# Kernel optimization log

Hardware: AMD Instinct MI355X
Metric: run time of the kernel (lower is better)

The kernel has to match this reference:

```python
import jax, jax.numpy as jnp
import numpy as np

B, C, H, W = 8, 64, 64, 64
DQK = C // 8  # q/k projection dim = 8


def setup_inputs() -> dict:
    key = jax.random.key(0)
    ks = jax.random.split(key, 5)
    return {
        "query": jax.random.normal(ks[0], (B, C, H, W), dtype=jnp.float32),
        "value": jax.random.normal(ks[1], (B, C, H, W), dtype=jnp.float32),
        "Wq": jax.random.normal(ks[2], (DQK, C), dtype=jnp.float32) * (1.0 / np.sqrt(C)),
        "bq": jnp.zeros((DQK,), dtype=jnp.float32),
        "Wk": jax.random.normal(ks[3], (DQK, C), dtype=jnp.float32) * (1.0 / np.sqrt(C)),
        "bk": jnp.zeros((DQK,), dtype=jnp.float32),
        "Wv": jax.random.normal(ks[4], (C, C), dtype=jnp.float32) * (1.0 / np.sqrt(C)),
        "bv": jnp.zeros((C,), dtype=jnp.float32),
    }


def reference(query, value, Wq, bq, Wk, bk, Wv, bv):
    b, c, h, w = value.shape
    n = h * w
    # 1x1 convs are per-pixel matmuls over channels
    q = jnp.einsum("oc,bchw->bohw", Wq, query) + bq[None, :, None, None]
    k = jnp.einsum("oc,bchw->bohw", Wk, query) + bk[None, :, None, None]
    v = jnp.einsum("oc,bchw->bohw", Wv, value) + bv[None, :, None, None]
    proj_q = q.reshape(b, DQK, n).transpose(0, 2, 1)  # [B, N, d]
    proj_k = k.reshape(b, DQK, n)                      # [B, d, N]
    energy = jnp.einsum("bnd,bdm->bnm", proj_q, proj_k)  # [B, N, N]
    attention = jax.nn.softmax(energy, axis=-1)
    proj_v = v.reshape(b, c, n)                        # [B, C, N]
    # out = proj_v @ attention^T
    out = jnp.einsum("bcm,bnm->bcn", proj_v, attention)
    out = out.reshape(b, c, h, w) + value
    return out
```

## Files before the change

### kernel.cpp

```cpp
#include <hip/hip_runtime.h>
#include <hip/hip_bf16.h>

typedef __attribute__((ext_vector_type(8))) __bf16 bf16x8;
typedef __attribute__((ext_vector_type(4))) float f32x4;

#if __has_builtin(__builtin_amdgcn_exp2f)
#define EXP2F(x) __builtin_amdgcn_exp2f(x)
#else
#define EXP2F(x) exp2f(x)
#endif

static constexpr int BB = 8, CC = 64, NN = 4096;
static constexpr size_t QF_OFF = 0;
static constexpr size_t KF_OFF = (size_t)2 << 20;
static constexpr size_t VF_OFF = (size_t)4 << 20;


__global__ __launch_bounds__(512) void proj_kernel(
    const float* __restrict__ query, const float* __restrict__ value,
    const float* __restrict__ Wq, const float* __restrict__ bq,
    const float* __restrict__ Wk, const float* __restrict__ bk,
    const float* __restrict__ Wv, const float* __restrict__ bv,
    char* __restrict__ ws) {
  __shared__ float qs[64][64];
  __shared__ float vvs[64][64];
  __shared__ __bf16 vlds[64][72];
  __shared__ float  qlds[64][9];
  __shared__ float  klds[64][9];
  const float LOG2E = 1.4426950408889634f;
  int t = threadIdx.x;
  int part = __builtin_amdgcn_readfirstlane(t >> 6);
  int px = t & 63;
  int blk = blockIdx.x;
  int b = blk >> 6;
  int px0 = (blk & 63) << 6;
  size_t inbase = (size_t)b * CC * NN + px0 + px;

  #pragma unroll
  for (int cc = 0; cc < 8; ++cc) {
    int c = part * 8 + cc;
    qs[c][px]  = query[inbase + (size_t)c * NN];
    vvs[c][px] = value[inbase + (size_t)c * NN];
  }
  __syncthreads();

  bool isq = part < 4;
  int qko = (part & 3) * 2;
  const float* __restrict__ Wqk = isq ? Wq : Wk;

  float vacc[8];
  #pragma unroll
  for (int o = 0; o < 8; ++o) vacc[o] = bv[part * 8 + o];
  float qk0 = 0.f, qk1 = 0.f;

  #pragma unroll
  for (int cb = 0; cb < 4; ++cb) {
    float xq[16], xv[16];
    #pragma unroll
    for (int cc = 0; cc < 16; ++cc) {
      xq[cc] = qs[cb * 16 + cc][px];
      xv[cc] = vvs[cb * 16 + cc][px];
    }
    #pragma unroll
    for (int cc = 0; cc < 16; ++cc) {
      int c = cb * 16 + cc;
      qk0 += Wqk[qko * 64 + c] * xq[cc];
      qk1 += Wqk[(qko + 1) * 64 + c] * xq[cc];
      #pragma unroll
      for (int o = 0; o < 8; ++o) vacc[o] += Wv[(part * 8 + o) * 64 + c] * xv[cc];
    }
  }

  #pragma unroll
  for (int o = 0; o < 8; ++o) vlds[px][part * 8 + o] = (__bf16)vacc[o];
  if (isq) {
    qlds[px][qko]     = (qk0 + bq[qko]) * LOG2E;
    qlds[px][qko + 1] = (qk1 + bq[qko + 1]) * LOG2E;
  } else {
    klds[px][qko]     = qk0 + bk[qko];
    klds[px][qko + 1] = qk1 + bk[qko + 1];
  }
  __syncthreads();

  __bf16* qfrag = (__bf16*)(ws + QF_OFF);
  __bf16* kfrag = (__bf16*)(ws + KF_OFF);
  __bf16* vfrag = (__bf16*)(ws + VF_OFF);
  int l = t & 63, cp = l & 15, qd = l >> 4;

  {
    int jt = t >> 8, ct = (t >> 6) & 3;
    bf16x8 v8;
    #pragma unroll
    for (int r = 0; r < 8; ++r) {
      int jj = (r < 4) ? (4 * qd + r) : (16 + 4 * qd + (r & 3));
      v8[r] = vlds[jt * 32 + jj][ct * 16 + cp];
    }
    int jtg = (blk & 63) * 2 + jt;
    *(bf16x8*)(vfrag + ((((size_t)b * 128 + jtg) * 4 + ct) * 64 + l) * 8) = v8;
  }
  if (t < 256) {
    int jt = t >> 7, th = (t >> 6) & 1;
    int pxl = jt * 32 + th * 16 + (l & 15);
    bf16x8 k8;
    #pragma unroll
    for (int r = 0; r < 8; ++r) {
      float kv = klds[pxl][r];
      __bf16 hi = (__bf16)kv;
      __bf16 lo = (__bf16)(kv - (float)hi);
      k8[r] = (qd < 2) ? hi : lo;
    }
    int jtg = (blk & 63) * 2 + jt;
    *(bf16x8*)(kfrag + ((((size_t)b * 128 + jtg) * 2 + th) * 64 + l) * 8) = k8;
  } else {
    int it = (t >> 6) & 3;
    int il = it * 16 + (l & 15);
    bf16x8 q8;
    #pragma unroll
    for (int r = 0; r < 8; ++r) {
      float qv = qlds[il][r];
      __bf16 hi = (__bf16)qv;
      __bf16 lo = (__bf16)(qv - (float)hi);
      q8[r] = ((qd & 1) == 0) ? hi : lo;
    }
    int itg = (blk & 63) * 4 + it;
    *(bf16x8*)(qfrag + (((size_t)b * 256 + itg) * 64 + l) * 8) = q8;
  }
}

__global__ __launch_bounds__(256, 2) void attn_kernel(
    const char* __restrict__ ws, const float* __restrict__ value,
    float* __restrict__ out) {
  __shared__ float lds_acc[32 * 4 * 64];
  __shared__ float lds_l[16 * 64];
  const __bf16* qfrag = (const __bf16*)(ws + QF_OFF);
  const __bf16* kfrag = (const __bf16*)(ws + KF_OFF);
  const __bf16* vfrag = (const __bf16*)(ws + VF_OFF);
  int tid = threadIdx.x;
  int w = tid >> 6, lane = tid & 63;
  int blk = blockIdx.x;
  int b = blk & 7;
  int slot = blk >> 3;
  int i0 = slot << 6;
  int itg0 = slot * 4;

  bf16x8 qf[4];
  #pragma unroll
  for (int it = 0; it < 4; ++it)
    qf[it] = *(const bf16x8*)(qfrag + (((size_t)b * 256 + itg0 + it) * 64 + lane) * 8);

  f32x4 acc[4][4];
  #pragma unroll
  for (int ct = 0; ct < 4; ++ct)
    #pragma unroll
    for (int it = 0; it < 4; ++it) acc[ct][it] = (f32x4){0.f, 0.f, 0.f, 0.f};
  float lsum[4] = {0.f, 0.f, 0.f, 0.f};

  const __bf16* kb = kfrag + (((size_t)b * 128 + w * 32) * 2 * 64 + lane) * 8;
  const __bf16* vb = vfrag + (((size_t)b * 128 + w * 32) * 4 * 64 + lane) * 8;

  auto compute = [&](bf16x8 kf0, bf16x8 kf1, bf16x8 vf0, bf16x8 vf1,
                     bf16x8 vf2, bf16x8 vf3) {
    const f32x4 z = (f32x4){0.f, 0.f, 0.f, 0.f};
    #pragma unroll
    for (int it = 0; it < 4; ++it) {
      f32x4 e0 = __builtin_amdgcn_mfma_f32_16x16x32_bf16(kf0, qf[it], z, 0, 0, 0);
      f32x4 e1 = __builtin_amdgcn_mfma_f32_16x16x32_bf16(kf1, qf[it], z, 0, 0, 0);
      bf16x8 pf;
      #pragma unroll
      for (int g = 0; g < 4; ++g) {
        float p0 = EXP2F(e0[g]); lsum[it] += p0; pf[g] = (__bf16)p0;
        float p1 = EXP2F(e1[g]); lsum[it] += p1; pf[4 + g] = (__bf16)p1;
      }
      acc[0][it] = __builtin_amdgcn_mfma_f32_16x16x32_bf16(vf0, pf, acc[0][it], 0, 0, 0);
      acc[1][it] = __builtin_amdgcn_mfma_f32_16x16x32_bf16(vf1, pf, acc[1][it], 0, 0, 0);
      acc[2][it] = __builtin_amdgcn_mfma_f32_16x16x32_bf16(vf2, pf, acc[2][it], 0, 0, 0);
      acc[3][it] = __builtin_amdgcn_mfma_f32_16x16x32_bf16(vf3, pf, acc[3][it], 0, 0, 0);
    }
  };

  bf16x8 k0a = *(const bf16x8*)(kb);
  bf16x8 k1a = *(const bf16x8*)(kb + 512);
  bf16x8 v0a = *(const bf16x8*)(vb);
  bf16x8 v1a = *(const bf16x8*)(vb + 512);
  bf16x8 v2a = *(const bf16x8*)(vb + 1024);
  bf16x8 v3a = *(const bf16x8*)(vb + 1536);

  #pragma unroll 1
  for (int itx = 0; itx < 16; ++itx) {
    kb += 1024; vb += 2048;
    bf16x8 k0b = *(const bf16x8*)(kb);
    bf16x8 k1b = *(const bf16x8*)(kb + 512);
    bf16x8 v0b = *(const bf16x8*)(vb);
    bf16x8 v1b = *(const bf16x8*)(vb + 512);
    bf16x8 v2b = *(const bf16x8*)(vb + 1024);
    bf16x8 v3b = *(const bf16x8*)(vb + 1536);
    compute(k0a, k1a, v0a, v1a, v2a, v3a);
    kb += 1024; vb += 2048;
    k0a = *(const bf16x8*)(kb);
    k1a = *(const bf16x8*)(kb + 512);
    v0a = *(const bf16x8*)(vb);
    v1a = *(const bf16x8*)(vb + 512);
    v2a = *(const bf16x8*)(vb + 1024);
    v3a = *(const bf16x8*)(vb + 1536);
    compute(k0b, k1b, v0b, v1b, v2b, v3b);
  }

  #pragma unroll
  for (int it = 0; it < 4; ++it) {
    lsum[it] += __shfl_xor(lsum[it], 16, 64);
    lsum[it] += __shfl_xor(lsum[it], 32, 64);
    lds_l[(it * 4 + w) * 64 + lane] = lsum[it];
  }

  int ect = tid >> 6, l = tid & 63;
  #pragma unroll
  for (int p = 0; p < 2; ++p) {
    if (p) __syncthreads();
    #pragma unroll
    for (int ct = 0; ct < 4; ++ct)
      #pragma unroll
      for (int itl = 0; itl < 2; ++itl)
        #pragma unroll
        for (int r = 0; r < 4; ++r) {
          int e = ct * 8 + itl * 4 + r;
          lds_acc[(e * 4 + w) * 64 + lane] = acc[ct][2 * p + itl][r];
        }
    __syncthreads();
    #pragma unroll
    for (int itl = 0; itl < 2; ++itl) {
      int it = 2 * p + itl;
      float ls = 0.f;
      #pragma unroll
      for (int ww = 0; ww < 4; ++ww) ls += lds_l[(it * 4 + ww) * 64 + (l & 15)];
      float inv = 1.0f / ls;
      int n = i0 + it * 16 + (l & 15);
      #pragma unroll
      for (int r = 0; r < 4; ++r) {
        int e = ect * 8 + itl * 4 + r;
        float s = 0.f;
        #pragma unroll
        for (int ww = 0; ww < 4; ++ww) s += lds_acc[(e * 4 + ww) * 64 + l];
        int c = ect * 16 + (l >> 4) * 4 + r;
        size_t idx = ((size_t)b * CC + c) * NN + n;
        out[idx] = s * inv + value[idx];
      }
    }
  }
}

extern "C" void kernel_launch(void* const* d_in, const int* in_sizes, int n_in,
                              void* d_out, int out_size, void* d_ws, size_t ws_size,
                              hipStream_t stream) {
  const float* query = (const float*)d_in[0];
  const float* value = (const float*)d_in[1];
  const float* Wq = (const float*)d_in[2];
  const float* bq = (const float*)d_in[3];
  const float* Wk = (const float*)d_in[4];
  const float* bk = (const float*)d_in[5];
  const float* Wv = (const float*)d_in[6];
  const float* bv = (const float*)d_in[7];
  float* out = (float*)d_out;

  proj_kernel<<<512, 512, 0, stream>>>(query, value, Wq, bq, Wk, bk, Wv, bv, (char*)d_ws);
  attn_kernel<<<512, 256, 0, stream>>>((const char*)d_ws, value, out);
}
```

Before: 124.0 us.

## Compute 1x1 projections with MFMA and vectorized float4 loads in proj_kernel

The Q/K/V projection kernel now uses 32x32x16 bf16 MFMA instead of scalar FMA loops. Inputs are staged into padded LDS with float4 global loads, and the block shrinks to 256 threads. Q/K precision is kept with a hi/lo bf16 split of both weights and inputs, while V is computed in plain bf16. This cuts ALU time in the projection stage but adds conversion work and some rounding error in V, and the attention kernel is left unchanged.

New measurement: 111.1 us. 10.4% less time.

```diff
diff --git a/kernel.cpp b/kernel.cpp
--- a/kernel.cpp
+++ b/kernel.cpp
@@ -3,6 +3,7 @@
 
 typedef __attribute__((ext_vector_type(8))) __bf16 bf16x8;
 typedef __attribute__((ext_vector_type(4))) float f32x4;
+typedef __attribute__((ext_vector_type(16))) float f32x16;
 
 #if __has_builtin(__builtin_amdgcn_exp2f)
 #define EXP2F(x) __builtin_amdgcn_exp2f(x)
@@ -16,79 +17,114 @@
 static constexpr size_t VF_OFF = (size_t)4 << 20;
 
 
-__global__ __launch_bounds__(512) void proj_kernel(
+__global__ __launch_bounds__(256, 2) void proj_kernel(
     const float* __restrict__ query, const float* __restrict__ value,
     const float* __restrict__ Wq, const float* __restrict__ bq,
     const float* __restrict__ Wk, const float* __restrict__ bk,
     const float* __restrict__ Wv, const float* __restrict__ bv,
     char* __restrict__ ws) {
-  __shared__ float qs[64][64];
-  __shared__ float vvs[64][64];
-  __shared__ __bf16 vlds[64][72];
+  __shared__ float xqs[64][68];
+  __shared__ float xvs[64][68];
+  __shared__ __bf16 vlds[64][66];
   __shared__ float  qlds[64][9];
   __shared__ float  klds[64][9];
   const float LOG2E = 1.4426950408889634f;
   int t = threadIdx.x;
-  int part = __builtin_amdgcn_readfirstlane(t >> 6);
-  int px = t & 63;
   int blk = blockIdx.x;
   int b = blk >> 6;
   int px0 = (blk & 63) << 6;
-  size_t inbase = (size_t)b * CC * NN + px0 + px;
-
-  #pragma unroll
-  for (int cc = 0; cc < 8; ++cc) {
-    int c = part * 8 + cc;
-    qs[c][px]  = query[inbase + (size_t)c * NN];
-    vvs[c][px] = value[inbase + (size_t)c * NN];
+
+  {
+    int c = t >> 2, seg = (t & 3) << 4;
+    size_t gaddr = (size_t)b * CC * NN + (size_t)c * NN + px0 + seg;
+    #pragma unroll
+    for (int qq = 0; qq < 4; ++qq) {
+      *(float4*)&xqs[c][seg + 4 * qq] = *(const float4*)(query + gaddr + 4 * qq);
+      *(float4*)&xvs[c][seg + 4 * qq] = *(const float4*)(value + gaddr + 4 * qq);
+    }
   }
   __syncthreads();
 
-  bool isq = part < 4;
-  int qko = (part & 3) * 2;
-  const float* __restrict__ Wqk = isq ? Wq : Wk;
-
-  float vacc[8];
-  #pragma unroll
-  for (int o = 0; o < 8; ++o) vacc[o] = bv[part * 8 + o];
-  float qk0 = 0.f, qk1 = 0.f;
-
-  #pragma unroll
-  for (int cb = 0; cb < 4; ++cb) {
-    float xq[16], xv[16];
-    #pragma unroll
-    for (int cc = 0; cc < 16; ++cc) {
-      xq[cc] = qs[cb * 16 + cc][px];
-      xv[cc] = vvs[cb * 16 + cc][px];
-    }
-    #pragma unroll
-    for (int cc = 0; cc < 16; ++cc) {
-      int c = cb * 16 + cc;
-      qk0 += Wqk[qko * 64 + c] * xq[cc];
-      qk1 += Wqk[(qko + 1) * 64 + c] * xq[cc];
-      #pragma unroll
-      for (int o = 0; o < 8; ++o) vacc[o] += Wv[(part * 8 + o) * 64 + c] * xv[cc];
-    }
-  }
-
-  #pragma unroll
-  for (int o = 0; o < 8; ++o) vlds[px][part * 8 + o] = (__bf16)vacc[o];
-  if (isq) {
-    qlds[px][qko]     = (qk0 + bq[qko]) * LOG2E;
-    qlds[px][qko + 1] = (qk1 + bq[qko + 1]) * LOG2E;
+  int lane = t & 63, m = lane & 31, hA = lane >> 5;
+  int w = t >> 6;
+  int tile = w & 1, role = w >> 1;
+  int pxl = tile * 32 + m;
+
+  f32x16 Z16;
+  #pragma unroll
+  for (int r = 0; r < 16; ++r) Z16[r] = 0.f;
+
+  if (role == 0) {
+    bf16x8 A[2][4];
+    #pragma unroll
+    for (int ct = 0; ct < 2; ++ct)
+      #pragma unroll
+      for (int kb = 0; kb < 4; ++kb) {
+        const float* wb = Wv + (ct * 32 + m) * 64 + kb * 16 + hA * 8;
+        #pragma unroll
+        for (int r = 0; r < 8; ++r) A[ct][kb][r] = (__bf16)wb[r];
+      }
+    f32x16 acc0 = Z16, acc1 = Z16;
+    #pragma unroll
+    for (int kb = 0; kb < 4; ++kb) {
+      bf16x8 Bv;
+      #pragma unroll
+      for (int r = 0; r < 8; ++r) Bv[r] = (__bf16)xvs[kb * 16 + hA * 8 + r][pxl];
+      acc0 = __builtin_amdgcn_mfma_f32_32x32x16_bf16(A[0][kb], Bv, acc0, 0, 0, 0);
+      acc1 = __builtin_amdgcn_mfma_f32_32x32x16_bf16(A[1][kb], Bv, acc1, 0, 0, 0);
+    }
+    #pragma unroll
+    for (int reg = 0; reg < 16; ++reg) {
+      int crow = (reg & 3) + 8 * (reg >> 2) + 4 * hA;
+      vlds[pxl][crow]      = (__bf16)(acc0[reg] + bv[crow]);
+      vlds[pxl][crow + 32] = (__bf16)(acc1[reg] + bv[crow + 32]);
+    }
   } else {
-    klds[px][qko]     = qk0 + bk[qko];
-    klds[px][qko + 1] = qk1 + bk[qko + 1];
+    bf16x8 A[4];
+    int r8 = m & 7;
+    bool isk = (m >> 3) & 1;
+    const float* wrow = (isk ? Wk : Wq) + r8 * 64;
+    float scale = isk ? 1.0f : LOG2E;
+    #pragma unroll
+    for (int kb = 0; kb < 4; ++kb) {
+      #pragma unroll
+      for (int r = 0; r < 8; ++r) {
+        float v = wrow[kb * 16 + hA * 8 + r] * scale;
+        __bf16 hi = (__bf16)v;
+        A[kb][r] = (m < 16) ? hi : (__bf16)(v - (float)hi);
+      }
+    }
+    f32x16 accH = Z16, accL = Z16;
+    #pragma unroll
+    for (int kb = 0; kb < 4; ++kb) {
+      bf16x8 Bh, Bl;
+      #pragma unroll
+      for (int r = 0; r < 8; ++r) {
+        float x = xqs[kb * 16 + hA * 8 + r][pxl];
+        __bf16 h = (__bf16)x;
+        Bh[r] = h;
+        Bl[r] = (__bf16)(x - (float)h);
+      }
+      accH = __builtin_amdgcn_mfma_f32_32x32x16_bf16(A[kb], Bh, accH, 0, 0, 0);
+      accL = __builtin_amdgcn_mfma_f32_32x32x16_bf16(A[kb], Bl, accL, 0, 0, 0);
+    }
+    #pragma unroll
+    for (int j = 0; j < 4; ++j) {
+      int o = 4 * hA + j;
+      qlds[pxl][o] = accH[j] + accH[8 + j] + accL[j] + bq[o] * LOG2E;
+      klds[pxl][o] = accH[4 + j] + accH[12 + j] + accL[4 + j] + bk[o];
+    }
   }
   __syncthreads();
 
   __bf16* qfrag = (__bf16*)(ws + QF_OFF);
   __bf16* kfrag = (__bf16*)(ws + KF_OFF);
   __bf16* vfrag = (__bf16*)(ws + VF_OFF);
-  int l = t & 63, cp = l & 15, qd = l >> 4;
-
-  {
-    int jt = t >> 8, ct = (t >> 6) & 3;
+  int l = lane, cp = l & 15, qd = l >> 4;
+
+  #pragma unroll
+  for (int ci = 0; ci < 2; ++ci) {
+    int jt = w >> 1, ct = (w & 1) * 2 + ci;
     bf16x8 v8;
     #pragma unroll
     for (int r = 0; r < 8; ++r) {
@@ -98,22 +134,22 @@
     int jtg = (blk & 63) * 2 + jt;
     *(bf16x8*)(vfrag + ((((size_t)b * 128 + jtg) * 4 + ct) * 64 + l) * 8) = v8;
   }
-  if (t < 256) {
-    int jt = t >> 7, th = (t >> 6) & 1;
-    int pxl = jt * 32 + th * 16 + (l & 15);
+  {
+    int jt = w >> 1, th = w & 1;
+    int pxk = jt * 32 + th * 16 + cp;
     bf16x8 k8;
     #pragma unroll
     for (int r = 0; r < 8; ++r) {
-      float kv = klds[pxl][r];
+      float kv = klds[pxk][r];
       __bf16 hi = (__bf16)kv;
       __bf16 lo = (__bf16)(kv - (float)hi);
       k8[r] = (qd < 2) ? hi : lo;
     }
     int jtg = (blk & 63) * 2 + jt;
     *(bf16x8*)(kfrag + ((((size_t)b * 128 + jtg) * 2 + th) * 64 + l) * 8) = k8;
-  } else {
-    int it = (t >> 6) & 3;
-    int il = it * 16 + (l & 15);
+  }
+  {
+    int il = w * 16 + cp;
     bf16x8 q8;
     #pragma unroll
     for (int r = 0; r < 8; ++r) {
@@ -122,7 +158,7 @@
       __bf16 lo = (__bf16)(qv - (float)hi);
       q8[r] = ((qd & 1) == 0) ? hi : lo;
     }
-    int itg = (blk & 63) * 4 + it;
+    int itg = (blk & 63) * 4 + w;
     *(bf16x8*)(qfrag + (((size_t)b * 256 + itg) * 64 + l) * 8) = q8;
   }
 }
@@ -261,6 +297,6 @@
   const float* bv = (const float*)d_in[7];
   float* out = (float*)d_out;
 
-  proj_kernel<<<512, 512, 0, stream>>>(query, value, Wq, bq, Wk, bk, Wv, bv, (char*)d_ws);
+  proj_kernel<<<512, 256, 0, stream>>>(query, value, Wq, bq, Wk, bk, Wv, bv, (char*)d_ws);
   attn_kernel<<<512, 256, 0, stream>>>((const char*)d_ws, value, out);
 }
```
